# Kernel optimization log

Measured on AMD Instinct MI355X. Metric: run time of the kernel, lower is better.

## Reference

```python
import jax, jax.numpy as jnp
import numpy as np

N_BINS = 15  # matches __init__ default


def setup_inputs() -> dict:
    key = jax.random.key(0)
    k1, k2 = jax.random.split(key)
    N, C = 100000, 1000
    softmaxes_probs = jax.random.uniform(k1, (N, C), dtype=jnp.float32)
    labels = jax.random.randint(k2, (N,), 0, C, dtype=jnp.int64)
    return {"softmaxes_probs": softmaxes_probs, "labels": labels}


def reference(softmaxes_probs, labels):
    # Classwise ECE: for each class c and bin b = (b/n_bins, (b+1)/n_bins],
    #   sce_c = sum_b |avg_conf_in_bin - acc_in_bin| * (count_in_bin / N)
    # returned value is mean_c sce_c.
    n_bins = N_BINS
    N, C = softmaxes_probs.shape
    conf = softmaxes_probs  # [N, C]

    # bin index: conf in (b/n_bins, (b+1)/n_bins] -> b ; conf <= 0 -> -1 (no bin)
    bin_idx = jnp.ceil(conf * n_bins).astype(jnp.int32) - 1
    bin_idx = jnp.minimum(bin_idx, n_bins - 1)
    valid = bin_idx >= 0

    class_ids = jnp.arange(C, dtype=jnp.int32)[None, :]  # [1, C]
    # combined segment id per (sample, class); invalid entries go to a dump segment
    seg = jnp.where(valid, bin_idx + class_ids * n_bins, C * n_bins)  # [N, C]
    seg_flat = seg.ravel()
    num_seg = C * n_bins + 1

    ones = jnp.ones_like(conf)
    counts = jax.ops.segment_sum(ones.ravel(), seg_flat, num_segments=num_seg)[:-1].reshape(C, n_bins)
    conf_sum = jax.ops.segment_sum(conf.ravel(), seg_flat, num_segments=num_seg)[:-1].reshape(C, n_bins)
    # labels_in_class broadcast to [N, C]
    correct = (labels[:, None] == jnp.arange(C, dtype=labels.dtype)[None, :]).astype(conf.dtype)
    correct_sum = jax.ops.segment_sum(correct.ravel(), seg_flat, num_segments=num_seg)[:-1].reshape(C, n_bins)

    prop_in_bin = counts / N  # prop_in_bin = in_bin.float().mean() over N samples
    nonempty = counts > 0
    denom = jnp.maximum(counts, 1.0)
    acc_in_bin = correct_sum / denom
    avg_conf_in_bin = conf_sum / denom
    contrib = jnp.where(nonempty, jnp.abs(avg_conf_in_bin - acc_in_bin) * prop_in_bin, 0.0)
    per_class_sce = jnp.sum(contrib, axis=1)  # [C]
    return jnp.mean(per_class_sce)
```

## Files before the change

kernel.cpp:

```cpp
#include <hip/hip_runtime.h>


#define NBINS   15
#define THREADS 512
#define CPT     2
#define TC      (THREADS * CPT)
#define PSTRIDE 31
#define LDSW    (THREADS * PSTRIDE)
#define SLAB    (TC * NBINS)
#define NGROUP  16

__global__ __launch_bounds__(THREADS, 4) void ece_hist(
    const float* __restrict__ probs, const int* __restrict__ labels,
    int N, int C, int R,
    int* __restrict__ partial)
{
    __shared__ unsigned sA[LDSW];
    const int t = threadIdx.x;
    #pragma unroll
    for (int i = t; i < LDSW; i += THREADS) sA[i] = 0u;
    __syncthreads();

    const int cls0 = 2 * t;
    const bool live = (cls0 + 1 < C);
    const int col  = live ? cls0 : 0;

    const int r0 = blockIdx.x * R;
    int rend = N - r0; if (rend > R) rend = R; if (rend < 0) rend = 0;

    const float2* p = (const float2*)(probs + (size_t)r0 * C + col);
    const size_t rowstep = (size_t)(C >> 1);
    unsigned* s0 = sA + t * PSTRIDE;

    float2 buf[8];
    int r = 0;
    for (; r + 8 <= rend; r += 8) {
        #pragma unroll
        for (int k = 0; k < 8; ++k)
            buf[k] = live ? p[(size_t)(r + k) * rowstep] : make_float2(0.f, 0.f);
        #pragma unroll
        for (int k = 0; k < 8; ++k) {
            float2 v = buf[k];
            int lab = labels[r0 + r + k];

            int b0 = (int)(v.x * 15.0f);
            b0 = b0 < NBINS - 1 ? b0 : NBINS - 1;
            unsigned c0 = (unsigned)fmaf(v.x, 65536.0f, 0.5f);
            c0 += (lab == cls0) ? (unsigned)(-65536) : 0u;
            atomicAdd(&s0[b0], (v.x > 0.0f) ? c0 : 0u);

            int b1 = (int)(v.y * 15.0f);
            b1 = b1 < NBINS - 1 ? b1 : NBINS - 1;
            unsigned c1 = (unsigned)fmaf(v.y, 65536.0f, 0.5f);
            c1 += (lab == cls0 + 1) ? (unsigned)(-65536) : 0u;
            atomicAdd(&s0[NBINS + b1], (v.y > 0.0f) ? c1 : 0u);
        }
    }
    for (; r < rend; ++r) {
        float2 v = live ? p[(size_t)r * rowstep] : make_float2(0.f, 0.f);
        int lab = labels[r0 + r];
        int b0 = (int)(v.x * 15.0f);
        b0 = b0 < NBINS - 1 ? b0 : NBINS - 1;
        unsigned c0 = (unsigned)fmaf(v.x, 65536.0f, 0.5f);
        c0 += (lab == cls0) ? (unsigned)(-65536) : 0u;
        atomicAdd(&s0[b0], (v.x > 0.0f) ? c0 : 0u);
        int b1 = (int)(v.y * 15.0f);
        b1 = b1 < NBINS - 1 ? b1 : NBINS - 1;
        unsigned c1 = (unsigned)fmaf(v.y, 65536.0f, 0.5f);
        c1 += (lab == cls0 + 1) ? (unsigned)(-65536) : 0u;
        atomicAdd(&s0[NBINS + b1], (v.y > 0.0f) ? c1 : 0u);
    }
    __syncthreads();

    int* dst = partial + (size_t)blockIdx.x * SLAB;
    #pragma unroll
    for (int i = t; i < SLAB; i += THREADS) {
        int owner = i / (2 * NBINS), j = i - owner * (2 * NBINS);
        dst[i] = (int)sA[owner * PSTRIDE + j];
    }
}

__global__ __launch_bounds__(256) void ece_red1(
    const int* __restrict__ partial, int chunks, int gsz,
    int* __restrict__ stage1, unsigned* __restrict__ counter)
{
    if (blockIdx.x == 0 && blockIdx.y == 0 && threadIdx.x == 0) *counter = 0u;
    int i = blockIdx.x * 256 + threadIdx.x;
    int g = blockIdx.y;
    int k0 = g * gsz;
    int k1 = k0 + gsz; if (k1 > chunks) k1 = chunks;
    int s = 0;
    #pragma unroll 8
    for (int k = k0; k < k1; ++k)
        s += partial[(size_t)k * SLAB + i];
    stage1[(size_t)g * SLAB + i] = s;
}

__global__ __launch_bounds__(256) void ece_red2(
    const int* __restrict__ stage1, int C, int N, int nb,
    float* __restrict__ blockSums, unsigned* __restrict__ counter,
    float* __restrict__ out)
{
    int i = blockIdx.x * 256 + threadIdx.x;
    float contrib = 0.0f;
    if (i < C * NBINS) {
        long long s = 0;
        #pragma unroll
        for (int g = 0; g < NGROUP; ++g)
            s += (long long)stage1[(size_t)g * SLAB + i];
        contrib = fabsf((float)s * (1.0f / 65536.0f)) * (1.0f / (float)N);
    }
    for (int o = 32; o; o >>= 1) contrib += __shfl_down(contrib, o);
    __shared__ float ws4[4];
    const int wid = threadIdx.x >> 6, lane = threadIdx.x & 63;
    if (lane == 0) ws4[wid] = contrib;
    __syncthreads();
    if (threadIdx.x == 0) {
        blockSums[blockIdx.x] = ws4[0] + ws4[1] + ws4[2] + ws4[3];
        __threadfence();
        unsigned old = atomicAdd(counter, 1u);
        if (old == (unsigned)(nb - 1)) {
            __threadfence();
            double s = 0.0;
            for (int b = 0; b < nb; ++b) s += (double)blockSums[b];
            out[0] = (float)(s / (double)C);
        }
    }
}

extern "C" void kernel_launch(void* const* d_in, const int* in_sizes, int n_in,
                              void* d_out, int out_size, void* d_ws, size_t ws_size,
                              hipStream_t stream) {
    const float* probs  = (const float*)d_in[0];
    const int*   labels = (const int*)d_in[1];
    const int N = in_sizes[1];
    const int C = in_sizes[0] / N;

    const size_t headBytes   = 4096;
    const size_t stage1Bytes = (size_t)NGROUP * SLAB * 4;
    const size_t off_partial = headBytes + stage1Bytes;
    const size_t slabBytes   = (size_t)SLAB * 4;

    unsigned* counter   = (unsigned*)d_ws;
    float*    blockSums = (float*)((char*)d_ws + 512);
    int*      stage1    = (int*)((char*)d_ws + headBytes);
    int*      partial   = (int*)((char*)d_ws + off_partial);

    long long avail = (long long)ws_size - (long long)off_partial;
    int chunks = (int)(avail / (long long)slabBytes);
    if (chunks > 500) chunks = 500;
    if (chunks < 4) chunks = 4;
    const int R   = (N + chunks - 1) / chunks;
    const int gsz = (chunks + NGROUP - 1) / NGROUP;
    const int nb2 = (C * NBINS + 255) / 256;

    ece_hist<<<chunks, THREADS, 0, stream>>>(probs, labels, N, C, R, partial);
    dim3 r1grid(SLAB / 256, NGROUP);
    ece_red1<<<r1grid, 256, 0, stream>>>(partial, chunks, gsz, stage1, counter);
    ece_red2<<<nb2, 256, 0, stream>>>(stage1, C, N, nb2, blockSums, counter,
                                      (float*)d_out);
}
```

Before: 99.46 us.

## Fuse two-stage reduction into one kernel with fixed-point atomic accumulation

The two reduction kernels (group partial sums, then a final sum over a stage1 buffer) become a single kernel. Each 1024-thread block sums its slot across all chunks in four quarter-groups, combines them in LDS, and adds a 40-bit fixed-point block sum into a 64-bit global atomic; the last block converts that to the output. This removes one kernel launch and the stage1 round trip through global memory. In exchange each reduction block does more serial work and the final sum is quantized to fixed point.

```diff
diff --git a/kernel.cpp b/kernel.cpp
--- a/kernel.cpp
+++ b/kernel.cpp
@@ -3,20 +3,23 @@
 
 #define NBINS   15
 #define THREADS 512
-#define CPT     2
-#define TC      (THREADS * CPT)
+#define TC      1024
 #define PSTRIDE 31
 #define LDSW    (THREADS * PSTRIDE)
 #define SLAB    (TC * NBINS)
-#define NGROUP  16
+#define SEGS    (SLAB / 256)
+#define Q40     1099511627776.0f
 
 __global__ __launch_bounds__(THREADS, 4) void ece_hist(
     const float* __restrict__ probs, const int* __restrict__ labels,
     int N, int C, int R,
-    int* __restrict__ partial)
+    int* __restrict__ partial,
+    unsigned long long* __restrict__ accum,
+    unsigned* __restrict__ doneCnt)
 {
     __shared__ unsigned sA[LDSW];
     const int t = threadIdx.x;
+    if (blockIdx.x == 0 && t == 0) { *accum = 0ull; *doneCnt = 0u; }
     #pragma unroll
     for (int i = t; i < LDSW; i += THREADS) sA[i] = 0u;
     __syncthreads();
@@ -80,50 +83,44 @@
     }
 }
 
-__global__ __launch_bounds__(256) void ece_red1(
-    const int* __restrict__ partial, int chunks, int gsz,
-    int* __restrict__ stage1, unsigned* __restrict__ counter)
+__global__ __launch_bounds__(1024, 1) void ece_red(
+    const int* __restrict__ partial, int chunks, int C, int N,
+    unsigned long long* __restrict__ accum, unsigned* __restrict__ doneCnt,
+    float* __restrict__ out)
 {
-    if (blockIdx.x == 0 && blockIdx.y == 0 && threadIdx.x == 0) *counter = 0u;
-    int i = blockIdx.x * 256 + threadIdx.x;
-    int g = blockIdx.y;
-    int k0 = g * gsz;
+    __shared__ int sq[4][256];
+    __shared__ float ws4[4];
+    const int t = threadIdx.x;
+    const int q = t >> 8, j = t & 255;
+    const int slot = blockIdx.x * 256 + j;
+
+    const int gsz = (chunks + 3) >> 2;
+    int k0 = q * gsz;
     int k1 = k0 + gsz; if (k1 > chunks) k1 = chunks;
     int s = 0;
     #pragma unroll 8
     for (int k = k0; k < k1; ++k)
-        s += partial[(size_t)k * SLAB + i];
-    stage1[(size_t)g * SLAB + i] = s;
-}
+        s += partial[(size_t)k * SLAB + slot];
+    sq[q][j] = s;
+    __syncthreads();
 
-__global__ __launch_bounds__(256) void ece_red2(
-    const int* __restrict__ stage1, int C, int N, int nb,
-    float* __restrict__ blockSums, unsigned* __restrict__ counter,
-    float* __restrict__ out)
-{
-    int i = blockIdx.x * 256 + threadIdx.x;
     float contrib = 0.0f;
-    if (i < C * NBINS) {
-        long long s = 0;
-        #pragma unroll
-        for (int g = 0; g < NGROUP; ++g)
-            s += (long long)stage1[(size_t)g * SLAB + i];
-        contrib = fabsf((float)s * (1.0f / 65536.0f)) * (1.0f / (float)N);
+    if (t < 256) {
+        long long tot = (long long)sq[0][t] + sq[1][t] + sq[2][t] + sq[3][t];
+        if (slot - j + t < C * NBINS)
+            contrib = fabsf((float)tot * (1.0f / 65536.0f)) * (1.0f / (float)N);
+        for (int o = 32; o; o >>= 1) contrib += __shfl_down(contrib, o);
+        if ((t & 63) == 0) ws4[t >> 6] = contrib;
     }
-    for (int o = 32; o; o >>= 1) contrib += __shfl_down(contrib, o);
-    __shared__ float ws4[4];
-    const int wid = threadIdx.x >> 6, lane = threadIdx.x & 63;
-    if (lane == 0) ws4[wid] = contrib;
     __syncthreads();
-    if (threadIdx.x == 0) {
-        blockSums[blockIdx.x] = ws4[0] + ws4[1] + ws4[2] + ws4[3];
+    if (t == 0) {
+        float bs = ws4[0] + ws4[1] + ws4[2] + ws4[3];
+        atomicAdd(accum, (unsigned long long)(bs * Q40));
         __threadfence();
-        unsigned old = atomicAdd(counter, 1u);
-        if (old == (unsigned)(nb - 1)) {
+        if (atomicAdd(doneCnt, 1u) == (unsigned)(SEGS - 1)) {
             __threadfence();
-            double s = 0.0;
-            for (int b = 0; b < nb; ++b) s += (double)blockSums[b];
-            out[0] = (float)(s / (double)C);
+            unsigned long long a = atomicAdd(accum, 0ull);
+            out[0] = (float)((double)a * (1.0 / (double)Q40) / (double)C);
         }
     }
 }
@@ -136,27 +133,21 @@
     const int N = in_sizes[1];
     const int C = in_sizes[0] / N;
 
-    const size_t headBytes   = 4096;
-    const size_t stage1Bytes = (size_t)NGROUP * SLAB * 4;
-    const size_t off_partial = headBytes + stage1Bytes;
-    const size_t slabBytes   = (size_t)SLAB * 4;
+    const size_t headBytes = 4096;
+    const size_t slabBytes = (size_t)SLAB * 4;
 
-    unsigned* counter   = (unsigned*)d_ws;
-    float*    blockSums = (float*)((char*)d_ws + 512);
-    int*      stage1    = (int*)((char*)d_ws + headBytes);
-    int*      partial   = (int*)((char*)d_ws + off_partial);
+    unsigned long long* accum   = (unsigned long long*)d_ws;
+    unsigned*           doneCnt = (unsigned*)((char*)d_ws + 8);
+    int*                partial = (int*)((char*)d_ws + headBytes);
 
-    long long avail = (long long)ws_size - (long long)off_partial;
+    long long avail = (long long)ws_size - (long long)headBytes;
     int chunks = (int)(avail / (long long)slabBytes);
-    if (chunks > 500) chunks = 500;
+    if (chunks > 512) chunks = 512;
     if (chunks < 4) chunks = 4;
-    const int R   = (N + chunks - 1) / chunks;
-    const int gsz = (chunks + NGROUP - 1) / NGROUP;
-    const int nb2 = (C * NBINS + 255) / 256;
+    const int R = (N + chunks - 1) / chunks;
 
-    ece_hist<<<chunks, THREADS, 0, stream>>>(probs, labels, N, C, R, partial);
-    dim3 r1grid(SLAB / 256, NGROUP);
-    ece_red1<<<r1grid, 256, 0, stream>>>(partial, chunks, gsz, stage1, counter);
-    ece_red2<<<nb2, 256, 0, stream>>>(stage1, C, N, nb2, blockSums, counter,
-                                      (float*)d_out);
+    ece_hist<<<chunks, THREADS, 0, stream>>>(probs, labels, N, C, R,
+                                             partial, accum, doneCnt);
+    ece_red<<<SEGS, 1024, 0, stream>>>(partial, chunks, C, N,
+                                       accum, doneCnt, (float*)d_out);
 }
```

After: 95.46 us. -4.0%, faster.
